# Performance work log

Hardware: AMD Instinct MI355X
Metric: run time of the kernel (lower is better)

Reference implementation:

```python
import jax, jax.numpy as jnp
import numpy as np

# Sizes (match init_kwargs / input_specs)
N, D, H, E = 4096, 512, 2048, 8   # tokens, dim, hidden_dim, num_experts
DK = 2                             # dynamic_k = top_k(3) - fixed_k(1)
NC = E - 1                         # dynamic candidate count (experts 1..7)
BETA_FIXED = 1.0 / 3.0             # fixed_k / top_k
BETA_DYN = 2.0 / 3.0               # dynamic_k / top_k


def setup_inputs() -> dict:
    key = jax.random.key(0)
    ks = jax.random.split(key, 5)
    def init(k, shape, fan_in):
        return jax.random.normal(k, shape, jnp.float32) * (1.0 / np.sqrt(fan_in))
    return {
        "x": jax.random.normal(ks[0], (N, D), jnp.float32),
        "router_W": init(ks[1], (D, NC), D),      # Linear(dim, num_non_fixed)
        "router_b": jnp.zeros((NC,), jnp.float32),
        "W1": init(ks[2], (E, D, H), D),           # per-expert first Linear
        "b1": jnp.zeros((E, H), jnp.float32),
        "W2": init(ks[3], (E, H, D), H),           # per-expert second Linear
        "b2": jnp.zeros((E, D), jnp.float32),
        "fixed_w": jnp.ones((1,), jnp.float32),    # fixed_branch_weights
    }


def reference(x, router_W, router_b, W1, b1, W2, b2, fixed_w):
    # All-expert MLP computed once (dense grouped-GEMM form of the
    # per-expert gather/MLP/scatter loop in the torch module).
    h = jax.nn.relu(jnp.einsum("nd,edh->neh", x, W1) + b1)   # [N,E,H]
    y = jnp.einsum("neh,ehd->ned", h, W2) + b2               # [N,E,D]

    # Fixed branch: expert 0 with fixed weight.
    fixed_out = fixed_w[0] * y[:, 0]                          # [N,D]

    # Dynamic branch: router over the 7 non-fixed experts.
    logits = x @ router_W + router_b                          # [N,NC]
    top_logits, top_idx = jax.lax.top_k(logits, DK)           # [N,DK]
    gates = jax.nn.softmax(top_logits, axis=-1)               # [N,DK]
    sel_expert = top_idx + 1                                  # lookup non_fixed [1..7]

    # combine weights per (token, expert): scatter gates via one-hot.
    combine = jnp.sum(jax.nn.one_hot(sel_expert, E, dtype=x.dtype)
                      * gates[..., None], axis=1)             # [N,E]
    dyn_out = jnp.einsum("ned,ne->nd", y, combine)            # [N,D]

    mixed = BETA_FIXED * fixed_out + BETA_DYN * dyn_out

    # Aux losses (same math as torch).
    importance = jax.nn.softmax(logits, axis=-1).mean(axis=0)  # [NC]
    uniform = 1.0 / NC
    load_balance_loss = jnp.mean((importance - uniform) ** 2)
    router_entropy = -jnp.sum(importance * jnp.log(jnp.clip(importance, 1e-8)))

    return mixed, load_balance_loss, router_entropy, sel_expert
```

## Files before the change

### kernel.cpp

```cpp
#include <hip/hip_runtime.h>
#include <math.h>

#define N_TOK 4096
#define DIM   512
#define HID   2048
#define NEXP  8
#define NC    7
#define OUT_MIXED (N_TOK*DIM)
#define TM    32

typedef __attribute__((ext_vector_type(8))) short bf16x8;
typedef __attribute__((ext_vector_type(4))) float f32x4;

#define XSP 520
#define HSP 264

#define OFF_XBF  262208ull
#define OFF_W1S  (OFF_XBF + 4194304ull)
#define OFF_W2S  (OFF_W1S + 16777216ull)
#define WS_REQ   (OFF_W2S + 16777216ull)

__device__ inline unsigned short f2bf(float f) {
  unsigned int u = __builtin_bit_cast(unsigned int, f);
  u = (u + 0x7fffu + ((u >> 16) & 1u)) >> 16;
  return (unsigned short)u;
}

__global__ __launch_bounds__(256) void router_kernel(
    const float* __restrict__ x, const float* __restrict__ rW,
    const float* __restrict__ rb, float* __restrict__ out,
    int* __restrict__ cpad, float* __restrict__ ipad,
    int* __restrict__ tok_list, float* __restrict__ wt_list)
{
  __shared__ float imp_loc[8];
  __shared__ int   cnt_loc[8];
  __shared__ int   ltok[8][32];
  __shared__ float lwt[8][32];
  __shared__ int   base_s[8];

  const int tid = threadIdx.x;
  if (tid < 8) { imp_loc[tid] = 0.f; cnt_loc[tid] = 0; }
  __syncthreads();
  const int wave = tid >> 6, lane = tid & 63;

  for (int it = 0; it < 4; ++it) {
    const int t = blockIdx.x * 16 + wave * 4 + it;
    float xv[8];
#pragma unroll
    for (int j = 0; j < 8; ++j) xv[j] = x[(size_t)t*DIM + lane + 64*j];
    float lg[NC];
#pragma unroll
    for (int e = 0; e < NC; ++e) {
      float s = 0.f;
#pragma unroll
      for (int j = 0; j < 8; ++j) s += xv[j] * rW[(lane + 64*j)*NC + e];
      lg[e] = s;
    }
#pragma unroll
    for (int e = 0; e < NC; ++e) {
      float s = lg[e];
#pragma unroll
      for (int off = 32; off > 0; off >>= 1) s += __shfl_xor(s, off, 64);
      lg[e] = s + rb[e];
    }
    int i1 = 0; float l1 = lg[0];
#pragma unroll
    for (int e = 1; e < NC; ++e) { if (lg[e] > l1) { l1 = lg[e]; i1 = e; } }
    int i2 = -1; float l2 = -3.4e38f;
#pragma unroll
    for (int e = 0; e < NC; ++e) { if (e != i1 && lg[e] > l2) { l2 = lg[e]; i2 = e; } }

    const float ed = expf(l2 - l1);
    const float g1 = 1.f/(1.f+ed), g2 = ed/(1.f+ed);

    float p[NC]; float ssum = 0.f;
#pragma unroll
    for (int e = 0; e < NC; ++e) { p[e] = expf(lg[e] - l1); ssum += p[e]; }
    const float inv = 1.f/ssum;

    if (lane == 0) {
#pragma unroll
      for (int e = 0; e < NC; ++e) atomicAdd(&imp_loc[e], p[e]*inv);
      out[OUT_MIXED + 2 + 2*t]     = (float)(i1 + 1);
      out[OUT_MIXED + 2 + 2*t + 1] = (float)(i2 + 1);
      const int e1 = i1 + 1, e2 = i2 + 1;
      int p1 = atomicAdd(&cnt_loc[e1], 1);
      ltok[e1][p1] = t;  lwt[e1][p1] = (2.f/3.f)*g1;
      int p2 = atomicAdd(&cnt_loc[e2], 1);
      ltok[e2][p2] = t;  lwt[e2][p2] = (2.f/3.f)*g2;
    }
  }
  __syncthreads();

  if (tid >= 1 && tid < 8)
    base_s[tid] = atomicAdd(&cpad[tid * 32], cnt_loc[tid]);
  if (tid < NC)
    atomicAdd(&ipad[(tid + 1) * 32], imp_loc[tid]);
  __syncthreads();

  {
    const int e = tid >> 5, i = tid & 31;
    if (e >= 1 && i < cnt_loc[e]) {
      const int dst = e * N_TOK + base_s[e] + i;
      tok_list[dst] = ltok[e][i];
      wt_list [dst] = lwt[e][i];
    }
  }
}

__global__ void finalize_kernel(const float* __restrict__ ipad,
                                float* __restrict__ out)
{
  if (threadIdx.x == 0 && blockIdx.x == 0) {
    float lb = 0.f, ent = 0.f;
    for (int e = 0; e < NC; ++e) {
      float p = ipad[(e + 1) * 32] * (1.f/(float)N_TOK);
      float d = p - (1.f/(float)NC);
      lb += d*d;
      ent -= p * logf(fmaxf(p, 1e-8f));
    }
    out[OUT_MIXED]     = lb * (1.f/(float)NC);
    out[OUT_MIXED + 1] = ent;
  }
}

__global__ __launch_bounds__(256) void convert_x(const float* __restrict__ x,
                                                 unsigned short* __restrict__ xbf)
{
  const int g = blockIdx.x * 256 + threadIdx.x;
  const float* src = x + (size_t)g * 8;
  unsigned short tmp[8];
#pragma unroll
  for (int j = 0; j < 8; ++j) tmp[j] = f2bf(src[j]);
  *(uint4*)(xbf + (size_t)g * 8) = *(const uint4*)tmp;
}

__global__ __launch_bounds__(256) void convert_w(
    const float* __restrict__ W, unsigned int* __restrict__ Ws,
    int K, int Nm, int tiles_n)
{
  __shared__ unsigned short lds[32][264];
  const int tid = threadIdx.x;
  const int b  = blockIdx.x;
  const int e  = b >> 7;
  const int rm = b & 127;
  const int tk = rm / tiles_n;
  const int tn = rm - tk * tiles_n;

  const float* src = W + ((size_t)e * K + tk * 32) * Nm + tn * 256;
#pragma unroll
  for (int it = 0; it < 32; ++it) {
    const int i = it * 256 + tid;
    const int row = i >> 8, col = i & 255;
    lds[row][col] = f2bf(src[(size_t)row * Nm + col]);
  }
  __syncthreads();

  const int ntiles = Nm >> 4, kblks = K >> 3;
#pragma unroll
  for (int it = 0; it < 16; ++it) {
    const int uid   = it * 256 + tid;
    const int nt_l  = uid >> 8;
    const int r     = uid & 255;
    const int kb_l  = r >> 6;
    const int u     = r & 63;
    const int n_lo  = u >> 2;
    const int k_hf  = u & 3;
    const int d_l   = kb_l * 8 + k_hf * 2;
    const int h_l   = nt_l * 16 + n_lo;
    const unsigned int s0 = lds[d_l][h_l], s1 = lds[d_l + 1][h_l];
    const int nt_g = tn * 16 + nt_l;
    const int kb_g = tk * 4 + kb_l;
    const size_t frag = ((size_t)e * ntiles + nt_g) * kblks + kb_g;
    Ws[frag * 64 + n_lo * 4 + k_hf] = s0 | (s1 << 16);
  }
}

__global__ __launch_bounds__(512) void moe_mlp_mfma(
    const unsigned short* __restrict__ xbf,
    const unsigned short* __restrict__ W1s,
    const unsigned short* __restrict__ W2s,
    const float* __restrict__ b1, const float* __restrict__ b2,
    const float* __restrict__ fixed_w,
    const int* __restrict__ cpad, const int* __restrict__ tok_list,
    const float* __restrict__ wt_list, float* __restrict__ out)
{
  const int e    = blockIdx.x >> 8;
  const int rest = blockIdx.x & 255;
  const int tile = rest >> 1;
  const int half = rest & 1;
  const int cnt  = (e == 0) ? N_TOK : cpad[e * 32];
  const int start = tile * TM;
  if (start >= cnt) return;

  __shared__ __align__(16) unsigned short xs[32 * XSP];
  __shared__ __align__(16) unsigned short hs[32 * HSP];
  __shared__ int   tok_s[TM];
  __shared__ float wt_s[TM];

  const int tid = threadIdx.x;
  if (tid < TM) {
    int idx = start + tid; int t = 0; float w = 0.f;
    if (idx < cnt) {
      if (e == 0) { t = idx; w = (1.f/3.f) * fixed_w[0]; }
      else        { t = tok_list[e*N_TOK + idx]; w = wt_list[e*N_TOK + idx]; }
    }
    tok_s[tid] = t; wt_s[tid] = w;
  }
  __syncthreads();

  for (int i = tid; i < 32 * 64; i += 512) {
    const int m = i >> 6, cb = i & 63;
    *(uint4*)(xs + m * XSP + cb * 8) =
        *(const uint4*)(xbf + (size_t)tok_s[m] * DIM + cb * 8);
  }

  const int lane = tid & 63;
  const int w    = tid >> 6;
  const int l15  = lane & 15;
  const int q    = lane >> 4;

  const unsigned short* W1e = W1s + (size_t)e * 128 * 64 * 128;
  const unsigned short* W2e = W2s + (size_t)e * 32 * 256 * 128;

  f32x4 yacc[2][4];
#pragma unroll
  for (int mi = 0; mi < 2; ++mi)
#pragma unroll
    for (int t = 0; t < 4; ++t) yacc[mi][t] = (f32x4){0.f, 0.f, 0.f, 0.f};

  __syncthreads();

  for (int c = half * 4; c < half * 4 + 4; ++c) {
    f32x4 hacc[2][2];
#pragma unroll
    for (int mi = 0; mi < 2; ++mi)
#pragma unroll
      for (int t = 0; t < 2; ++t) hacc[mi][t] = (f32x4){0.f, 0.f, 0.f, 0.f};
    const int nt_base = c * 16 + w * 2;
#pragma unroll 4
    for (int s = 0; s < 16; ++s) {
      const bf16x8 a0 = *(const bf16x8*)(xs + l15 * XSP + s * 32 + q * 8);
      const bf16x8 a1 = *(const bf16x8*)(xs + (16 + l15) * XSP + s * 32 + q * 8);
#pragma unroll
      for (int t = 0; t < 2; ++t) {
        const bf16x8 b = *(const bf16x8*)(
            W1e + (((size_t)(nt_base + t) * 64) + s * 4 + q) * 128 + l15 * 8);
        hacc[0][t] = __builtin_amdgcn_mfma_f32_16x16x32_bf16(a0, b, hacc[0][t], 0, 0, 0);
        hacc[1][t] = __builtin_amdgcn_mfma_f32_16x16x32_bf16(a1, b, hacc[1][t], 0, 0, 0);
      }
    }
#pragma unroll
    for (int t = 0; t < 2; ++t) {
      const float bv = b1[e * HID + (nt_base + t) * 16 + l15];
      const int col = w * 32 + t * 16 + l15;
#pragma unroll
      for (int reg = 0; reg < 4; ++reg) {
        hs[(q * 4 + reg) * HSP + col]      = f2bf(fmaxf(hacc[0][t][reg] + bv, 0.f));
        hs[(16 + q * 4 + reg) * HSP + col] = f2bf(fmaxf(hacc[1][t][reg] + bv, 0.f));
      }
    }
    __syncthreads();

#pragma unroll 2
    for (int s = 0; s < 8; ++s) {
      const bf16x8 a0 = *(const bf16x8*)(hs + l15 * HSP + s * 32 + q * 8);
      const bf16x8 a1 = *(const bf16x8*)(hs + (16 + l15) * HSP + s * 32 + q * 8);
      const int kblk = c * 32 + s * 4 + q;
#pragma unroll
      for (int t = 0; t < 4; ++t) {
        const bf16x8 b = *(const bf16x8*)(
            W2e + (((size_t)(w * 4 + t) * 256) + kblk) * 128 + l15 * 8);
        yacc[0][t] = __builtin_amdgcn_mfma_f32_16x16x32_bf16(a0, b, yacc[0][t], 0, 0, 0);
        yacc[1][t] = __builtin_amdgcn_mfma_f32_16x16x32_bf16(a1, b, yacc[1][t], 0, 0, 0);
      }
    }
    __syncthreads();
  }

#pragma unroll
  for (int t = 0; t < 4; ++t) {
    const int d = (w * 4 + t) * 16 + l15;
    const float b2v = half ? 0.f : b2[e * DIM + d];
#pragma unroll
    for (int reg = 0; reg < 4; ++reg) {
      const int m0 = q * 4 + reg, m1 = 16 + q * 4 + reg;
      atomicAdd(&out[(size_t)tok_s[m0] * DIM + d], wt_s[m0] * (yacc[0][t][reg] + b2v));
      atomicAdd(&out[(size_t)tok_s[m1] * DIM + d], wt_s[m1] * (yacc[1][t][reg] + b2v));
    }
  }
}

__global__ __launch_bounds__(256) void moe_mlp_kernel(
    const float* __restrict__ x,
    const float* __restrict__ W1, const float* __restrict__ b1,
    const float* __restrict__ W2, const float* __restrict__ b2,
    const float* __restrict__ fixed_w,
    const int* __restrict__ cpad, const int* __restrict__ tok_list,
    const float* __restrict__ wt_list, float* __restrict__ out)
{
  const int e    = blockIdx.x >> 8;
  const int tile = blockIdx.x & 255;
  const int cnt  = (e == 0) ? N_TOK : cpad[e * 32];
  const int start = tile * 16;
  if (start >= cnt) return;

  __shared__ float xs[DIM][17];
  __shared__ float hs2[256][17];
  __shared__ int   tok_s[16];
  __shared__ float wt_s[16];

  const int tid = threadIdx.x;
  if (tid < 16) {
    int idx = start + tid; int t = 0; float w = 0.f;
    if (idx < cnt) {
      if (e == 0) { t = idx; w = (1.f/3.f) * fixed_w[0]; }
      else        { t = tok_list[e*N_TOK + idx]; w = wt_list[e*N_TOK + idx]; }
    }
    tok_s[tid] = t; wt_s[tid] = w;
  }
  __syncthreads();

  for (int i = tid; i < 16*DIM; i += 256) {
    const int m = i >> 9, d = i & (DIM-1);
    xs[d][m] = x[(size_t)tok_s[m]*DIM + d];
  }

  const int r  = tid & 63;
  const int m0 = (tid >> 6) * 4;
  const float* W1e = W1 + (size_t)e * DIM * HID;
  const float* W2e = W2 + (size_t)e * HID * DIM;
  const float* b1e = b1 + e * HID;

  float yacc[4][8];
#pragma unroll
  for (int j = 0; j < 4; ++j)
#pragma unroll
    for (int i = 0; i < 8; ++i) yacc[j][i] = 0.f;

  __syncthreads();

  for (int c = 0; c < 8; ++c) {
    const int k0 = c * 256;
    float bv[4];
#pragma unroll
    for (int i = 0; i < 4; ++i) bv[i] = b1e[k0 + r + 64*i];
    float hacc[4][4];
#pragma unroll
    for (int j = 0; j < 4; ++j)
#pragma unroll
      for (int i = 0; i < 4; ++i) hacc[j][i] = bv[i];
#pragma unroll 2
    for (int d = 0; d < DIM; ++d) {
      float wv[4];
#pragma unroll
      for (int i = 0; i < 4; ++i) wv[i] = W1e[(size_t)d*HID + k0 + r + 64*i];
      float xv[4];
#pragma unroll
      for (int j = 0; j < 4; ++j) xv[j] = xs[d][m0+j];
#pragma unroll
      for (int j = 0; j < 4; ++j)
#pragma unroll
        for (int i = 0; i < 4; ++i) hacc[j][i] += xv[j]*wv[i];
    }
#pragma unroll
    for (int i = 0; i < 4; ++i)
#pragma unroll
      for (int j = 0; j < 4; ++j) hs2[r + 64*i][m0+j] = fmaxf(hacc[j][i], 0.f);
    __syncthreads();

#pragma unroll 2
    for (int k = 0; k < 256; ++k) {
      float wv2[8];
#pragma unroll
      for (int i = 0; i < 8; ++i) wv2[i] = W2e[(size_t)(k0+k)*DIM + r + 64*i];
      float hv[4];
#pragma unroll
      for (int j = 0; j < 4; ++j) hv[j] = hs2[k][m0+j];
#pragma unroll
      for (int j = 0; j < 4; ++j)
#pragma unroll
        for (int i = 0; i < 8; ++i) yacc[j][i] += hv[j]*wv2[i];
    }
    __syncthreads();
  }

#pragma unroll
  for (int i = 0; i < 8; ++i) {
    const int d = r + 64*i;
    const float b2v = b2[e*DIM + d];
#pragma unroll
    for (int j = 0; j < 4; ++j) {
      const int m = m0 + j;
      atomicAdd(&out[(size_t)tok_s[m]*DIM + d], wt_s[m]*(yacc[j][i] + b2v));
    }
  }
}

extern "C" void kernel_launch(void* const* d_in, const int* in_sizes, int n_in,
                              void* d_out, int out_size, void* d_ws, size_t ws_size,
                              hipStream_t stream)
{
  const float* x  = (const float*)d_in[0];
  const float* rW = (const float*)d_in[1];
  const float* rb = (const float*)d_in[2];
  const float* W1 = (const float*)d_in[3];
  const float* b1 = (const float*)d_in[4];
  const float* W2 = (const float*)d_in[5];
  const float* b2 = (const float*)d_in[6];
  const float* fw = (const float*)d_in[7];
  float* out = (float*)d_out;

  int*   tok_list = (int*)((char*)d_ws + 64);
  float* wt_list  = (float*)((char*)d_ws + 64 + (size_t)NEXP*N_TOK*4);
  int*   cpad     = tok_list;
  float* ipad     = wt_list;

  hipMemsetAsync(cpad, 0, 1024, stream);
  hipMemsetAsync(ipad, 0, 1024, stream);
  hipMemsetAsync(d_out, 0, (size_t)OUT_MIXED*4, stream);

  router_kernel<<<256, 256, 0, stream>>>(x, rW, rb, out, cpad, ipad,
                                         tok_list, wt_list);
  finalize_kernel<<<1, 64, 0, stream>>>(ipad, out);

  if (ws_size >= WS_REQ) {
    unsigned short* xbf = (unsigned short*)((char*)d_ws + OFF_XBF);
    unsigned int*   W1s = (unsigned int*)((char*)d_ws + OFF_W1S);
    unsigned int*   W2s = (unsigned int*)((char*)d_ws + OFF_W2S);
    convert_x<<<1024, 256, 0, stream>>>(x, xbf);
    convert_w<<<1024, 256, 0, stream>>>(W1, W1s, DIM, HID, 8);
    convert_w<<<1024, 256, 0, stream>>>(W2, W2s, HID, DIM, 2);
    moe_mlp_mfma<<<NEXP*256, 512, 0, stream>>>(xbf, (const unsigned short*)W1s,
                                               (const unsigned short*)W2s, b1, b2, fw,
                                               cpad, tok_list, wt_list, out);
  } else {
    moe_mlp_kernel<<<NEXP*256, 256, 0, stream>>>(x, W1, b1, W2, b2, fw,
                                                 cpad, tok_list, wt_list, out);
  }
}
```

Measured before the change: 271.3 us.

## Fuse prep kernels, enlarge MFMA token tile, and rebalance expert block scheduling

Merges the router, finalize, x/W bf16 conversions and output zeroing into a single prep kernel. The loss finalize now runs in the last router block, chosen by an atomic counter. The MoE MFMA kernel doubles the token tile from 32 to 64 rows, so each weight fragment is reused across four M sub-tiles, and it sets launch bounds for two blocks per CU. A new block-index mapping interleaves expert-0 and dynamic-expert work units to balance the grid and cut empty blocks. This trades fewer launches and better weight reuse for more registers and LDS per block. It also puts a grid-wide atomic completion check in the prep kernel.

```diff
diff --git a/kernel.cpp b/kernel.cpp
--- a/kernel.cpp
+++ b/kernel.cpp
@@ -7,7 +7,7 @@
 #define NEXP  8
 #define NC    7
 #define OUT_MIXED (N_TOK*DIM)
-#define TM    32
+#define TM    64
 
 typedef __attribute__((ext_vector_type(8))) short bf16x8;
 typedef __attribute__((ext_vector_type(4))) float f32x4;
@@ -26,126 +26,16 @@
   return (unsigned short)u;
 }
 
-__global__ __launch_bounds__(256) void router_kernel(
-    const float* __restrict__ x, const float* __restrict__ rW,
-    const float* __restrict__ rb, float* __restrict__ out,
-    int* __restrict__ cpad, float* __restrict__ ipad,
-    int* __restrict__ tok_list, float* __restrict__ wt_list)
-{
-  __shared__ float imp_loc[8];
-  __shared__ int   cnt_loc[8];
-  __shared__ int   ltok[8][32];
-  __shared__ float lwt[8][32];
-  __shared__ int   base_s[8];
-
-  const int tid = threadIdx.x;
-  if (tid < 8) { imp_loc[tid] = 0.f; cnt_loc[tid] = 0; }
-  __syncthreads();
-  const int wave = tid >> 6, lane = tid & 63;
-
-  for (int it = 0; it < 4; ++it) {
-    const int t = blockIdx.x * 16 + wave * 4 + it;
-    float xv[8];
-#pragma unroll
-    for (int j = 0; j < 8; ++j) xv[j] = x[(size_t)t*DIM + lane + 64*j];
-    float lg[NC];
-#pragma unroll
-    for (int e = 0; e < NC; ++e) {
-      float s = 0.f;
-#pragma unroll
-      for (int j = 0; j < 8; ++j) s += xv[j] * rW[(lane + 64*j)*NC + e];
-      lg[e] = s;
-    }
-#pragma unroll
-    for (int e = 0; e < NC; ++e) {
-      float s = lg[e];
-#pragma unroll
-      for (int off = 32; off > 0; off >>= 1) s += __shfl_xor(s, off, 64);
-      lg[e] = s + rb[e];
-    }
-    int i1 = 0; float l1 = lg[0];
-#pragma unroll
-    for (int e = 1; e < NC; ++e) { if (lg[e] > l1) { l1 = lg[e]; i1 = e; } }
-    int i2 = -1; float l2 = -3.4e38f;
-#pragma unroll
-    for (int e = 0; e < NC; ++e) { if (e != i1 && lg[e] > l2) { l2 = lg[e]; i2 = e; } }
-
-    const float ed = expf(l2 - l1);
-    const float g1 = 1.f/(1.f+ed), g2 = ed/(1.f+ed);
-
-    float p[NC]; float ssum = 0.f;
-#pragma unroll
-    for (int e = 0; e < NC; ++e) { p[e] = expf(lg[e] - l1); ssum += p[e]; }
-    const float inv = 1.f/ssum;
-
-    if (lane == 0) {
-#pragma unroll
-      for (int e = 0; e < NC; ++e) atomicAdd(&imp_loc[e], p[e]*inv);
-      out[OUT_MIXED + 2 + 2*t]     = (float)(i1 + 1);
-      out[OUT_MIXED + 2 + 2*t + 1] = (float)(i2 + 1);
-      const int e1 = i1 + 1, e2 = i2 + 1;
-      int p1 = atomicAdd(&cnt_loc[e1], 1);
-      ltok[e1][p1] = t;  lwt[e1][p1] = (2.f/3.f)*g1;
-      int p2 = atomicAdd(&cnt_loc[e2], 1);
-      ltok[e2][p2] = t;  lwt[e2][p2] = (2.f/3.f)*g2;
-    }
-  }
-  __syncthreads();
-
-  if (tid >= 1 && tid < 8)
-    base_s[tid] = atomicAdd(&cpad[tid * 32], cnt_loc[tid]);
-  if (tid < NC)
-    atomicAdd(&ipad[(tid + 1) * 32], imp_loc[tid]);
-  __syncthreads();
-
-  {
-    const int e = tid >> 5, i = tid & 31;
-    if (e >= 1 && i < cnt_loc[e]) {
-      const int dst = e * N_TOK + base_s[e] + i;
-      tok_list[dst] = ltok[e][i];
-      wt_list [dst] = lwt[e][i];
-    }
-  }
-}
-
-__global__ void finalize_kernel(const float* __restrict__ ipad,
-                                float* __restrict__ out)
-{
-  if (threadIdx.x == 0 && blockIdx.x == 0) {
-    float lb = 0.f, ent = 0.f;
-    for (int e = 0; e < NC; ++e) {
-      float p = ipad[(e + 1) * 32] * (1.f/(float)N_TOK);
-      float d = p - (1.f/(float)NC);
-      lb += d*d;
-      ent -= p * logf(fmaxf(p, 1e-8f));
-    }
-    out[OUT_MIXED]     = lb * (1.f/(float)NC);
-    out[OUT_MIXED + 1] = ent;
-  }
-}
-
-__global__ __launch_bounds__(256) void convert_x(const float* __restrict__ x,
-                                                 unsigned short* __restrict__ xbf)
-{
-  const int g = blockIdx.x * 256 + threadIdx.x;
-  const float* src = x + (size_t)g * 8;
-  unsigned short tmp[8];
-#pragma unroll
-  for (int j = 0; j < 8; ++j) tmp[j] = f2bf(src[j]);
-  *(uint4*)(xbf + (size_t)g * 8) = *(const uint4*)tmp;
-}
-
-__global__ __launch_bounds__(256) void convert_w(
-    const float* __restrict__ W, unsigned int* __restrict__ Ws,
-    int K, int Nm, int tiles_n)
-{
-  __shared__ unsigned short lds[32][264];
-  const int tid = threadIdx.x;
-  const int b  = blockIdx.x;
-  const int e  = b >> 7;
-  const int rm = b & 127;
-  const int tk = rm / tiles_n;
-  const int tn = rm - tk * tiles_n;
+template<int K, int Nm, int TILES_N>
+__device__ void convert_w_body(const float* __restrict__ W,
+                               unsigned int* __restrict__ Ws,
+                               int blk, int tid,
+                               unsigned short lds[32][264])
+{
+  const int e  = blk >> 7;
+  const int rm = blk & 127;
+  const int tk = rm / TILES_N;
+  const int tn = rm - tk * TILES_N;
 
   const float* src = W + ((size_t)e * K + tk * 32) * Nm + tn * 256;
 #pragma unroll
@@ -176,7 +66,131 @@
   }
 }
 
-__global__ __launch_bounds__(512) void moe_mlp_mfma(
+__global__ __launch_bounds__(256) void prep_kernel(
+    const float* __restrict__ x, const float* __restrict__ rW,
+    const float* __restrict__ rb, float* __restrict__ out,
+    int* __restrict__ cpad, float* __restrict__ ipad,
+    int* __restrict__ tok_list, float* __restrict__ wt_list,
+    unsigned short* __restrict__ xbf,
+    const float* __restrict__ W1, unsigned int* __restrict__ W1s,
+    const float* __restrict__ W2, unsigned int* __restrict__ W2s)
+{
+  __shared__ unsigned short clds[32][264];
+  __shared__ float imp_loc[8];
+  __shared__ int   cnt_loc[8];
+  __shared__ int   ltok[8][32];
+  __shared__ float lwt[8][32];
+  __shared__ int   base_s[8];
+
+  const int b   = blockIdx.x;
+  const int tid = threadIdx.x;
+
+  if (b < 1024) {
+    const int g = b * 256 + tid;
+    const float* src = x + (size_t)g * 8;
+    unsigned short tmp[8];
+#pragma unroll
+    for (int j = 0; j < 8; ++j) tmp[j] = f2bf(src[j]);
+    *(uint4*)(xbf + (size_t)g * 8) = *(const uint4*)tmp;
+    return;
+  }
+  if (b < 2048) { convert_w_body< 512, 2048, 8>(W1, W1s, b - 1024, tid, clds); return; }
+  if (b < 3072) { convert_w_body<2048,  512, 2>(W2, W2s, b - 2048, tid, clds); return; }
+
+  const int rb_ = b - 3072;
+
+  {
+    const float4 z = {0.f, 0.f, 0.f, 0.f};
+    float4* o4 = (float4*)out + (size_t)rb_ * 2048;
+    for (int i = tid; i < 2048; i += 256) o4[i] = z;
+  }
+
+  if (tid < 8) { imp_loc[tid] = 0.f; cnt_loc[tid] = 0; }
+  __syncthreads();
+  const int wave = tid >> 6, lane = tid & 63;
+
+  for (int it = 0; it < 4; ++it) {
+    const int t = rb_ * 16 + wave * 4 + it;
+    float xv[8];
+#pragma unroll
+    for (int j = 0; j < 8; ++j) xv[j] = x[(size_t)t*DIM + lane + 64*j];
+    float lg[NC];
+#pragma unroll
+    for (int e = 0; e < NC; ++e) {
+      float s = 0.f;
+#pragma unroll
+      for (int j = 0; j < 8; ++j) s += xv[j] * rW[(lane + 64*j)*NC + e];
+      lg[e] = s;
+    }
+#pragma unroll
+    for (int e = 0; e < NC; ++e) {
+      float s = lg[e];
+#pragma unroll
+      for (int off = 32; off > 0; off >>= 1) s += __shfl_xor(s, off, 64);
+      lg[e] = s + rb[e];
+    }
+    int i1 = 0; float l1 = lg[0];
+#pragma unroll
+    for (int e = 1; e < NC; ++e) { if (lg[e] > l1) { l1 = lg[e]; i1 = e; } }
+    int i2 = -1; float l2 = -3.4e38f;
+#pragma unroll
+    for (int e = 0; e < NC; ++e) { if (e != i1 && lg[e] > l2) { l2 = lg[e]; i2 = e; } }
+
+    const float ed = expf(l2 - l1);
+    const float g1 = 1.f/(1.f+ed), g2 = ed/(1.f+ed);
+
+    float p[NC]; float ssum = 0.f;
+#pragma unroll
+    for (int e = 0; e < NC; ++e) { p[e] = expf(lg[e] - l1); ssum += p[e]; }
+    const float inv = 1.f/ssum;
+
+    if (lane == 0) {
+#pragma unroll
+      for (int e = 0; e < NC; ++e) atomicAdd(&imp_loc[e], p[e]*inv);
+      out[OUT_MIXED + 2 + 2*t]     = (float)(i1 + 1);
+      out[OUT_MIXED + 2 + 2*t + 1] = (float)(i2 + 1);
+      const int e1 = i1 + 1, e2 = i2 + 1;
+      int p1 = atomicAdd(&cnt_loc[e1], 1);
+      ltok[e1][p1] = t;  lwt[e1][p1] = (2.f/3.f)*g1;
+      int p2 = atomicAdd(&cnt_loc[e2], 1);
+      ltok[e2][p2] = t;  lwt[e2][p2] = (2.f/3.f)*g2;
+    }
+  }
+  __syncthreads();
+
+  if (tid >= 1 && tid < 8)
+    base_s[tid] = atomicAdd(&cpad[tid * 32], cnt_loc[tid]);
+  if (tid < NC)
+    atomicAdd(&ipad[(tid + 1) * 32], imp_loc[tid]);
+  __syncthreads();
+
+  {
+    const int e = tid >> 5, i = tid & 31;
+    if (e >= 1 && i < cnt_loc[e]) {
+      const int dst = e * N_TOK + base_s[e] + i;
+      tok_list[dst] = ltok[e][i];
+      wt_list [dst] = lwt[e][i];
+    }
+  }
+
+  __threadfence();
+  __syncthreads();
+  if (tid == 0) {
+    if (atomicAdd(&cpad[0], 1) == 255) {
+      float lb = 0.f, ent = 0.f;
+      for (int ee = 0; ee < NC; ++ee) {
+        float p = atomicAdd(&ipad[(ee + 1) * 32], 0.f) * (1.f/(float)N_TOK);
+        float d = p - (1.f/(float)NC);
+        lb += d*d;
+        ent -= p * logf(fmaxf(p, 1e-8f));
+      }
+      out[OUT_MIXED]     = lb * (1.f/(float)NC);
+      out[OUT_MIXED + 1] = ent;
+    }
+  }
+}
+
+__global__ __launch_bounds__(512, 2) void moe_mlp_mfma(
     const unsigned short* __restrict__ xbf,
     const unsigned short* __restrict__ W1s,
     const unsigned short* __restrict__ W2s,
@@ -185,31 +199,43 @@
     const int* __restrict__ cpad, const int* __restrict__ tok_list,
     const float* __restrict__ wt_list, float* __restrict__ out)
 {
-  const int e    = blockIdx.x >> 8;
-  const int rest = blockIdx.x & 255;
-  const int tile = rest >> 1;
-  const int half = rest & 1;
-  const int cnt  = (e == 0) ? N_TOK : cpad[e * 32];
+  const int b = blockIdx.x;
+  int e, tile, half;
+  if (b < 256) {
+    const int rho = b & 7, u = b >> 3;
+    const int quota = (rho < 6) ? 11 : 31;
+    if (u >= quota) return;
+    const int prefix = (rho < 6) ? rho * 11 : (rho == 6 ? 66 : 97);
+    const int unit = prefix + u;
+    e = 0; half = unit >> 6; tile = unit & 63;
+  } else {
+    const int v = b - 256;
+    const int rho = v & 7, u = v >> 3;
+    const int cls = ((u >> 6) << 3) + rho;
+    if (cls >= 14) return;
+    e = (cls >> 1) + 1; half = cls & 1; tile = u & 63;
+  }
+  const int cnt   = (e == 0) ? N_TOK : cpad[e * 32];
   const int start = tile * TM;
   if (start >= cnt) return;
 
-  __shared__ __align__(16) unsigned short xs[32 * XSP];
-  __shared__ __align__(16) unsigned short hs[32 * HSP];
+  __shared__ __align__(16) unsigned short xs[TM * XSP];
+  __shared__ __align__(16) unsigned short hs[TM * HSP];
   __shared__ int   tok_s[TM];
   __shared__ float wt_s[TM];
 
   const int tid = threadIdx.x;
   if (tid < TM) {
-    int idx = start + tid; int t = 0; float w = 0.f;
+    int idx = start + tid; int t = 0; float wv = 0.f;
     if (idx < cnt) {
-      if (e == 0) { t = idx; w = (1.f/3.f) * fixed_w[0]; }
-      else        { t = tok_list[e*N_TOK + idx]; w = wt_list[e*N_TOK + idx]; }
-    }
-    tok_s[tid] = t; wt_s[tid] = w;
-  }
-  __syncthreads();
-
-  for (int i = tid; i < 32 * 64; i += 512) {
+      if (e == 0) { t = idx; wv = (1.f/3.f) * fixed_w[0]; }
+      else        { t = tok_list[e*N_TOK + idx]; wv = wt_list[e*N_TOK + idx]; }
+    }
+    tok_s[tid] = t; wt_s[tid] = wv;
+  }
+  __syncthreads();
+
+  for (int i = tid; i < TM * 64; i += 512) {
     const int m = i >> 6, cb = i & 63;
     *(uint4*)(xs + m * XSP + cb * 8) =
         *(const uint4*)(xbf + (size_t)tok_s[m] * DIM + cb * 8);
@@ -223,31 +249,34 @@
   const unsigned short* W1e = W1s + (size_t)e * 128 * 64 * 128;
   const unsigned short* W2e = W2s + (size_t)e * 32 * 256 * 128;
 
-  f32x4 yacc[2][4];
-#pragma unroll
-  for (int mi = 0; mi < 2; ++mi)
+  f32x4 yacc[4][4];
+#pragma unroll
+  for (int mi = 0; mi < 4; ++mi)
 #pragma unroll
     for (int t = 0; t < 4; ++t) yacc[mi][t] = (f32x4){0.f, 0.f, 0.f, 0.f};
 
   __syncthreads();
 
   for (int c = half * 4; c < half * 4 + 4; ++c) {
-    f32x4 hacc[2][2];
-#pragma unroll
-    for (int mi = 0; mi < 2; ++mi)
+    f32x4 hacc[4][2];
+#pragma unroll
+    for (int mi = 0; mi < 4; ++mi)
 #pragma unroll
       for (int t = 0; t < 2; ++t) hacc[mi][t] = (f32x4){0.f, 0.f, 0.f, 0.f};
     const int nt_base = c * 16 + w * 2;
 #pragma unroll 4
     for (int s = 0; s < 16; ++s) {
-      const bf16x8 a0 = *(const bf16x8*)(xs + l15 * XSP + s * 32 + q * 8);
-      const bf16x8 a1 = *(const bf16x8*)(xs + (16 + l15) * XSP + s * 32 + q * 8);
+      bf16x8 a[4];
+#pragma unroll
+      for (int mi = 0; mi < 4; ++mi)
+        a[mi] = *(const bf16x8*)(xs + (mi*16 + l15) * XSP + s * 32 + q * 8);
 #pragma unroll
       for (int t = 0; t < 2; ++t) {
-        const bf16x8 b = *(const bf16x8*)(
+        const bf16x8 bb = *(const bf16x8*)(
             W1e + (((size_t)(nt_base + t) * 64) + s * 4 + q) * 128 + l15 * 8);
-        hacc[0][t] = __builtin_amdgcn_mfma_f32_16x16x32_bf16(a0, b, hacc[0][t], 0, 0, 0);
-        hacc[1][t] = __builtin_amdgcn_mfma_f32_16x16x32_bf16(a1, b, hacc[1][t], 0, 0, 0);
+#pragma unroll
+        for (int mi = 0; mi < 4; ++mi)
+          hacc[mi][t] = __builtin_amdgcn_mfma_f32_16x16x32_bf16(a[mi], bb, hacc[mi][t], 0, 0, 0);
       }
     }
 #pragma unroll
@@ -255,24 +284,28 @@
       const float bv = b1[e * HID + (nt_base + t) * 16 + l15];
       const int col = w * 32 + t * 16 + l15;
 #pragma unroll
-      for (int reg = 0; reg < 4; ++reg) {
-        hs[(q * 4 + reg) * HSP + col]      = f2bf(fmaxf(hacc[0][t][reg] + bv, 0.f));
-        hs[(16 + q * 4 + reg) * HSP + col] = f2bf(fmaxf(hacc[1][t][reg] + bv, 0.f));
-      }
+      for (int mi = 0; mi < 4; ++mi)
+#pragma unroll
+        for (int reg = 0; reg < 4; ++reg)
+          hs[(mi*16 + q*4 + reg) * HSP + col] =
+              f2bf(fmaxf(hacc[mi][t][reg] + bv, 0.f));
     }
     __syncthreads();
 
 #pragma unroll 2
     for (int s = 0; s < 8; ++s) {
-      const bf16x8 a0 = *(const bf16x8*)(hs + l15 * HSP + s * 32 + q * 8);
-      const bf16x8 a1 = *(const bf16x8*)(hs + (16 + l15) * HSP + s * 32 + q * 8);
+      bf16x8 a[4];
+#pragma unroll
+      for (int mi = 0; mi < 4; ++mi)
+        a[mi] = *(const bf16x8*)(hs + (mi*16 + l15) * HSP + s * 32 + q * 8);
       const int kblk = c * 32 + s * 4 + q;
 #pragma unroll
       for (int t = 0; t < 4; ++t) {
-        const bf16x8 b = *(const bf16x8*)(
+        const bf16x8 bb = *(const bf16x8*)(
             W2e + (((size_t)(w * 4 + t) * 256) + kblk) * 128 + l15 * 8);
-        yacc[0][t] = __builtin_amdgcn_mfma_f32_16x16x32_bf16(a0, b, yacc[0][t], 0, 0, 0);
-        yacc[1][t] = __builtin_amdgcn_mfma_f32_16x16x32_bf16(a1, b, yacc[1][t], 0, 0, 0);
+#pragma unroll
+        for (int mi = 0; mi < 4; ++mi)
+          yacc[mi][t] = __builtin_amdgcn_mfma_f32_16x16x32_bf16(a[mi], bb, yacc[mi][t], 0, 0, 0);
       }
     }
     __syncthreads();
@@ -283,11 +316,110 @@
     const int d = (w * 4 + t) * 16 + l15;
     const float b2v = half ? 0.f : b2[e * DIM + d];
 #pragma unroll
-    for (int reg = 0; reg < 4; ++reg) {
-      const int m0 = q * 4 + reg, m1 = 16 + q * 4 + reg;
-      atomicAdd(&out[(size_t)tok_s[m0] * DIM + d], wt_s[m0] * (yacc[0][t][reg] + b2v));
-      atomicAdd(&out[(size_t)tok_s[m1] * DIM + d], wt_s[m1] * (yacc[1][t][reg] + b2v));
-    }
+    for (int mi = 0; mi < 4; ++mi)
+#pragma unroll
+      for (int reg = 0; reg < 4; ++reg) {
+        const int m = mi*16 + q*4 + reg;
+        atomicAdd(&out[(size_t)tok_s[m] * DIM + d], wt_s[m] * (yacc[mi][t][reg] + b2v));
+      }
+  }
+}
+
+__global__ __launch_bounds__(256) void router_kernel(
+    const float* __restrict__ x, const float* __restrict__ rW,
+    const float* __restrict__ rb, float* __restrict__ out,
+    int* __restrict__ cpad, float* __restrict__ ipad,
+    int* __restrict__ tok_list, float* __restrict__ wt_list)
+{
+  __shared__ float imp_loc[8];
+  __shared__ int   cnt_loc[8];
+  __shared__ int   ltok[8][32];
+  __shared__ float lwt[8][32];
+  __shared__ int   base_s[8];
+
+  const int tid = threadIdx.x;
+  if (tid < 8) { imp_loc[tid] = 0.f; cnt_loc[tid] = 0; }
+  __syncthreads();
+  const int wave = tid >> 6, lane = tid & 63;
+
+  for (int it = 0; it < 4; ++it) {
+    const int t = blockIdx.x * 16 + wave * 4 + it;
+    float xv[8];
+#pragma unroll
+    for (int j = 0; j < 8; ++j) xv[j] = x[(size_t)t*DIM + lane + 64*j];
+    float lg[NC];
+#pragma unroll
+    for (int e = 0; e < NC; ++e) {
+      float s = 0.f;
+#pragma unroll
+      for (int j = 0; j < 8; ++j) s += xv[j] * rW[(lane + 64*j)*NC + e];
+      lg[e] = s;
+    }
+#pragma unroll
+    for (int e = 0; e < NC; ++e) {
+      float s = lg[e];
+#pragma unroll
+      for (int off = 32; off > 0; off >>= 1) s += __shfl_xor(s, off, 64);
+      lg[e] = s + rb[e];
+    }
+    int i1 = 0; float l1 = lg[0];
+#pragma unroll
+    for (int e = 1; e < NC; ++e) { if (lg[e] > l1) { l1 = lg[e]; i1 = e; } }
+    int i2 = -1; float l2 = -3.4e38f;
+#pragma unroll
+    for (int e = 0; e < NC; ++e) { if (e != i1 && lg[e] > l2) { l2 = lg[e]; i2 = e; } }
+
+    const float ed = expf(l2 - l1);
+    const float g1 = 1.f/(1.f+ed), g2 = ed/(1.f+ed);
+
+    float p[NC]; float ssum = 0.f;
+#pragma unroll
+    for (int e = 0; e < NC; ++e) { p[e] = expf(lg[e] - l1); ssum += p[e]; }
+    const float inv = 1.f/ssum;
+
+    if (lane == 0) {
+#pragma unroll
+      for (int e = 0; e < NC; ++e) atomicAdd(&imp_loc[e], p[e]*inv);
+      out[OUT_MIXED + 2 + 2*t]     = (float)(i1 + 1);
+      out[OUT_MIXED + 2 + 2*t + 1] = (float)(i2 + 1);
+      const int e1 = i1 + 1, e2 = i2 + 1;
+      int p1 = atomicAdd(&cnt_loc[e1], 1);
+      ltok[e1][p1] = t;  lwt[e1][p1] = (2.f/3.f)*g1;
+      int p2 = atomicAdd(&cnt_loc[e2], 1);
+      ltok[e2][p2] = t;  lwt[e2][p2] = (2.f/3.f)*g2;
+    }
+  }
+  __syncthreads();
+
+  if (tid >= 1 && tid < 8)
+    base_s[tid] = atomicAdd(&cpad[tid * 32], cnt_loc[tid]);
+  if (tid < NC)
+    atomicAdd(&ipad[(tid + 1) * 32], imp_loc[tid]);
+  __syncthreads();
+
+  {
+    const int e = tid >> 5, i = tid & 31;
+    if (e >= 1 && i < cnt_loc[e]) {
+      const int dst = e * N_TOK + base_s[e] + i;
+      tok_list[dst] = ltok[e][i];
+      wt_list [dst] = lwt[e][i];
+    }
+  }
+}
+
+__global__ void finalize_kernel(const float* __restrict__ ipad,
+                                float* __restrict__ out)
+{
+  if (threadIdx.x == 0 && blockIdx.x == 0) {
+    float lb = 0.f, ent = 0.f;
+    for (int e = 0; e < NC; ++e) {
+      float p = ipad[(e + 1) * 32] * (1.f/(float)N_TOK);
+      float d = p - (1.f/(float)NC);
+      lb += d*d;
+      ent -= p * logf(fmaxf(p, 1e-8f));
+    }
+    out[OUT_MIXED]     = lb * (1.f/(float)NC);
+    out[OUT_MIXED + 1] = ent;
   }
 }
 
@@ -414,27 +546,25 @@
   int*   tok_list = (int*)((char*)d_ws + 64);
   float* wt_list  = (float*)((char*)d_ws + 64 + (size_t)NEXP*N_TOK*4);
   int*   cpad     = tok_list;
-  float* ipad     = wt_list;
-
-  hipMemsetAsync(cpad, 0, 1024, stream);
-  hipMemsetAsync(ipad, 0, 1024, stream);
-  hipMemsetAsync(d_out, 0, (size_t)OUT_MIXED*4, stream);
-
-  router_kernel<<<256, 256, 0, stream>>>(x, rW, rb, out, cpad, ipad,
-                                         tok_list, wt_list);
-  finalize_kernel<<<1, 64, 0, stream>>>(ipad, out);
+  float* ipad     = (float*)((char*)tok_list + 1024);
+
+  hipMemsetAsync(cpad, 0, 2048, stream);
 
   if (ws_size >= WS_REQ) {
     unsigned short* xbf = (unsigned short*)((char*)d_ws + OFF_XBF);
     unsigned int*   W1s = (unsigned int*)((char*)d_ws + OFF_W1S);
     unsigned int*   W2s = (unsigned int*)((char*)d_ws + OFF_W2S);
-    convert_x<<<1024, 256, 0, stream>>>(x, xbf);
-    convert_w<<<1024, 256, 0, stream>>>(W1, W1s, DIM, HID, 8);
-    convert_w<<<1024, 256, 0, stream>>>(W2, W2s, HID, DIM, 2);
-    moe_mlp_mfma<<<NEXP*256, 512, 0, stream>>>(xbf, (const unsigned short*)W1s,
-                                               (const unsigned short*)W2s, b1, b2, fw,
-                                               cpad, tok_list, wt_list, out);
+    prep_kernel<<<3328, 256, 0, stream>>>(x, rW, rb, out, cpad, ipad,
+                                          tok_list, wt_list, xbf,
+                                          W1, W1s, W2, W2s);
+    moe_mlp_mfma<<<1280, 512, 0, stream>>>(xbf, (const unsigned short*)W1s,
+                                           (const unsigned short*)W2s, b1, b2, fw,
+                                           cpad, tok_list, wt_list, out);
   } else {
+    hipMemsetAsync(d_out, 0, (size_t)OUT_MIXED*4, stream);
+    router_kernel<<<256, 256, 0, stream>>>(x, rW, rb, out, cpad, ipad,
+                                           tok_list, wt_list);
+    finalize_kernel<<<1, 64, 0, stream>>>(ipad, out);
     moe_mlp_kernel<<<NEXP*256, 256, 0, stream>>>(x, W1, b1, W2, b2, fw,
                                                  cpad, tok_list, wt_list, out);
   }
```

Result: slower. 311.4 us (+14.8%).
